# Kernel optimization log

Measured on AMD Instinct MI355X. Metric: run time of the kernel, lower is better.

The kernel has to match this reference:

```python
import jax, jax.numpy as jnp
import numpy as np

EMA_BETA = 0.9
NUM_HEADS = 16

def causal_prefix_ema(x, beta):
    # x: [b, t, d]; s_t = beta*s_{t-1} + (1-beta)*x_t, s_{-1}=0
    def step(s, xt):
        s = beta * s + (1.0 - beta) * xt
        return s, s
    s0 = jnp.zeros_like(x[:, 0, :])
    _, ys = jax.lax.scan(step, s0, jnp.swapaxes(x, 0, 1))  # [t, b, d]
    return jnp.swapaxes(ys, 0, 1)

def setup_inputs() -> dict:
    key = jax.random.key(0)
    ks = jax.random.split(key, 9)
    b, t, d = 2, 1024, 2048
    sc = lambda fan_in: 1.0 / np.sqrt(fan_in)
    return {
        "x": jax.random.normal(ks[0], (b, t, d), jnp.float32),
        "l3_memory": jax.random.normal(ks[1], (b, 1, d), jnp.float32),
        "wq": jax.random.normal(ks[2], (d, d), jnp.float32) * sc(d),
        "wk": jax.random.normal(ks[3], (d, d), jnp.float32) * sc(d),
        "wv": jax.random.normal(ks[4], (d, d), jnp.float32) * sc(d),
        "wo": jax.random.normal(ks[5], (d, d), jnp.float32) * sc(d),
        "rw1": jax.random.normal(ks[6], (d // 2, d), jnp.float32) * sc(d),
        "rb1": jnp.zeros((d // 2,), jnp.float32),
        "rw2": jax.random.normal(ks[7], (3, d // 2), jnp.float32) * sc(d // 2),
        "rb2": jnp.zeros((3,), jnp.float32),
    }

def reference(x, l3_memory, wq, wk, wv, wo, rw1, rb1, rw2, rb2):
    b, t, d = x.shape
    h = NUM_HEADS
    dh = d // h
    scale = 1.0 / np.sqrt(dh)

    q = x @ wq.T                                   # [b,t,d]
    l1 = x
    l2 = causal_prefix_ema(x, EMA_BETA)            # [b,t,d]
    l3 = jnp.broadcast_to(l3_memory, (b, t, d))    # repeat retrieval memory to length t

    # router: MLP(Q) -> softmax over 3 levels
    hdn = jax.nn.silu(q @ rw1.T + rb1)
    lam = jax.nn.softmax(hdn @ rw2.T + rb2, axis=-1)  # [b,t,3]

    fused = lam[..., 0:1] * l1 + lam[..., 1:2] * l2 + lam[..., 2:3] * l3

    def heads(y):
        return jnp.swapaxes(y.reshape(b, t, h, dh), 1, 2)  # [b,h,t,dh]

    qh = heads(q)
    kh = heads(fused @ wk.T)
    vh = heads(fused @ wv.T)

    scores = jnp.einsum("bhqd,bhkd->bhqk", qh, kh) * scale
    causal = jnp.tril(jnp.ones((t, t), bool))
    scores = jnp.where(causal, scores, jnp.finfo(scores.dtype).min)
    attn = jax.nn.softmax(scores, axis=-1)
    out = jnp.einsum("bhqk,bhkd->bhqd", attn, vh)

    out = jnp.swapaxes(out, 1, 2).reshape(b, t, d) @ wo.T
    return (out, kh, vh, lam)
```

## Files before the change

kernel.cpp:

```cpp
#include <hip/hip_runtime.h>
#include <hip/hip_bf16.h>
#include <math.h>

#define B_  2
#define T_  1024
#define D_  2048
#define H_  16
#define DH_ 128
#define M_  2048
#define DR_ 1024
#define CH_  16
#define NCH_ 64

typedef __attribute__((ext_vector_type(8))) short short8;
typedef __attribute__((ext_vector_type(4))) short sh4;
typedef __attribute__((ext_vector_type(4))) float f32x4;

__device__ __forceinline__ void gld16(const __hip_bfloat16* g, __hip_bfloat16* l) {
  __builtin_amdgcn_global_load_lds(
      (const __attribute__((address_space(1))) unsigned int*)g,
      (__attribute__((address_space(3))) unsigned int*)l, 16, 0, 0);
}

template<int BM, int CMODE, bool SILU>
__global__ __launch_bounds__(256)
void gemm_mfma(const __hip_bfloat16* __restrict__ A,
               const __hip_bfloat16* __restrict__ Bm,
               const float* __restrict__ bias,
               float* __restrict__ C, __hip_bfloat16* __restrict__ Cb,
               float* __restrict__ C2, __hip_bfloat16* __restrict__ Cb2,
               int M, int N, int K)
{
  constexpr int NI = BM / 32;
  constexpr int AC = BM / 64;
  __shared__ __hip_bfloat16 As[2][2][BM * 32];
  __shared__ __hip_bfloat16 Bs[2][2][128 * 32];
  const int tid  = threadIdx.x;
  const int wave = tid >> 6;
  const int lane = tid & 63;
  const int m0 = blockIdx.y * BM;
  const int n0 = blockIdx.x * 128;
  const int wm = (wave >> 1) * (BM / 2);
  const int wn = (wave & 1) * 64;

  const int srow = lane >> 2;
  const int scol = (lane & 3) * 8;
  const __hip_bfloat16* Ag = A  + (size_t)(m0 + wave * (BM / 4) + srow) * K + scol;
  const __hip_bfloat16* Bg = Bm + (size_t)(n0 + wave * 32 + srow) * K + scol;

  const int fr = lane & 15;
  const int fk = (lane >> 4) * 8;

  f32x4 acc[NI][4];
  #pragma unroll
  for (int i = 0; i < NI; ++i)
    #pragma unroll
    for (int j = 0; j < 4; ++j) acc[i][j] = (f32x4)0.f;

  auto stage = [&](int bf, int k0) {
    #pragma unroll
    for (int h = 0; h < 2; ++h) {
      #pragma unroll
      for (int c = 0; c < AC; ++c)
        gld16(Ag + k0 + h * 32 + (size_t)(c * 16) * K,
              &As[bf][h][(wave * (BM / 4) + c * 16) * 32]);
      #pragma unroll
      for (int c = 0; c < 2; ++c)
        gld16(Bg + k0 + h * 32 + (size_t)(c * 16) * K,
              &Bs[bf][h][(wave * 32 + c * 16) * 32]);
    }
  };

  stage(0, 0);
  __syncthreads();
  int cur = 0;
  for (int k0 = 0; k0 < K; k0 += 64) {
    if (k0 + 64 < K) stage(cur ^ 1, k0 + 64);
    #pragma unroll
    for (int h = 0; h < 2; ++h) {
      short8 af[NI], bfr[4];
      #pragma unroll
      for (int i = 0; i < NI; ++i)
        af[i]  = *(const short8*)&As[cur][h][(wm + i * 16 + fr) * 32 + fk];
      #pragma unroll
      for (int j = 0; j < 4; ++j)
        bfr[j] = *(const short8*)&Bs[cur][h][(wn + j * 16 + fr) * 32 + fk];
      #pragma unroll
      for (int i = 0; i < NI; ++i)
        #pragma unroll
        for (int j = 0; j < 4; ++j)
          acc[i][j] = __builtin_amdgcn_mfma_f32_16x16x32_bf16(af[i], bfr[j], acc[i][j], 0, 0, 0);
    }
    __syncthreads();
    cur ^= 1;
  }

  #pragma unroll
  for (int i = 0; i < NI; ++i) {
    #pragma unroll
    for (int j = 0; j < 4; ++j) {
      const int row0 = m0 + wm + i * 16 + (lane >> 4) * 4;
      const int col  = n0 + wn + j * 16 + (lane & 15);
      float vr[4];
      #pragma unroll
      for (int r = 0; r < 4; ++r) {
        float v = acc[i][j][r];
        if (bias) v += bias[col];
        if (SILU) v = v / (1.f + __expf(-v));
        vr[r] = v;
      }
      if (CMODE == 0) {
        #pragma unroll
        for (int r = 0; r < 4; ++r) C[(size_t)(row0 + r) * N + col] = vr[r];
      } else if (CMODE == 1) {
        #pragma unroll
        for (int r = 0; r < 4; ++r) Cb[(size_t)(row0 + r) * N + col] = __float2bfloat16(vr[r]);
      } else {
        const int bb = row0 >> 10, t0v = row0 & 1023;
        if (col < D_) {
          const int hh = col >> 7, dd = col & 127;
          #pragma unroll
          for (int r = 0; r < 4; ++r) {
            const size_t idx = (((size_t)(bb * H_ + hh)) * T_ + t0v + r) * DH_ + dd;
            C[idx] = vr[r];
            Cb[idx] = __float2bfloat16(vr[r]);
          }
        } else {
          const int c2 = col - D_;
          const int hh = c2 >> 7, dd = c2 & 127;
          #pragma unroll
          for (int r = 0; r < 4; ++r)
            C2[(((size_t)(bb * H_ + hh)) * T_ + t0v + r) * DH_ + dd] = vr[r];
          __hip_bfloat16 tmp[4];
          #pragma unroll
          for (int r = 0; r < 4; ++r) tmp[r] = __float2bfloat16(vr[r]);
          *(sh4*)(Cb2 + (((size_t)(bb * H_ + hh)) * DH_ + dd) * T_ + t0v) = *(const sh4*)tmp;
        }
      }
    }
  }
}

__global__ __launch_bounds__(256)
void prep_all(const float* __restrict__ x, __hip_bfloat16* __restrict__ xb,
              float* __restrict__ l2, float* __restrict__ lf,
              const float* __restrict__ s1, const float* __restrict__ s2,
              const float* __restrict__ s3, const float* __restrict__ s4,
              const float* __restrict__ s5,
              __hip_bfloat16* d1, __hip_bfloat16* d2, __hip_bfloat16* d3,
              __hip_bfloat16* d4, __hip_bfloat16* d5,
              int n1, int n2, int n3, int n4, int n5)
{
  if (blockIdx.y == 0) {
    const int bid = blockIdx.x;
    if (bid >= 256) return;
    const int dblk = bid & 1;
    const int ch   = (bid >> 1) & 63;
    const int b    = bid >> 7;
    const int t0 = ch * CH_;
    const int d  = dblk * 1024 + threadIdx.x * 4;
    const float* xp = x  + (size_t)b * T_ * D_ + d;
    float*       lp = l2 + (size_t)b * T_ * D_ + d;
    __hip_bfloat16* xo = xb + (size_t)b * T_ * D_ + d;
    float4 s = make_float4(0.f, 0.f, 0.f, 0.f);
    #pragma unroll 4
    for (int t = t0; t < t0 + CH_; ++t) {
      float4 v = *(const float4*)(xp + (size_t)t * D_);
      __hip_bfloat16 tmp[4] = {__float2bfloat16(v.x), __float2bfloat16(v.y),
                               __float2bfloat16(v.z), __float2bfloat16(v.w)};
      *(sh4*)(xo + (size_t)t * D_) = *(const sh4*)tmp;
      s.x = 0.9f * s.x + 0.1f * v.x;
      s.y = 0.9f * s.y + 0.1f * v.y;
      s.z = 0.9f * s.z + 0.1f * v.z;
      s.w = 0.9f * s.w + 0.1f * v.w;
      *(float4*)(lp + (size_t)t * D_) = s;
    }
    *(float4*)(lf + ((size_t)b * NCH_ + ch) * D_ + d) = s;
    return;
  }
  const float* s; __hip_bfloat16* d; int n;
  switch (blockIdx.y) {
    case 1: s = s1; d = d1; n = n1; break;
    case 2: s = s2; d = d2; n = n2; break;
    case 3: s = s3; d = d3; n = n3; break;
    case 4: s = s4; d = d4; n = n4; break;
    default: s = s5; d = d5; n = n5; break;
  }
  const int i = (blockIdx.x * 256 + threadIdx.x) * 8;
  if (i < n) {
    float4 a = *(const float4*)(s + i);
    float4 b = *(const float4*)(s + i + 4);
    __hip_bfloat16 t[8] = {__float2bfloat16(a.x), __float2bfloat16(a.y),
                           __float2bfloat16(a.z), __float2bfloat16(a.w),
                           __float2bfloat16(b.x), __float2bfloat16(b.y),
                           __float2bfloat16(b.z), __float2bfloat16(b.w)};
    *(short8*)(d + i) = *(const short8*)t;
  }
}

__global__ __launch_bounds__(256)
void ema_carry_scan(const float* __restrict__ lf, float* __restrict__ carry)
{
  const int wid  = (blockIdx.x * 256 + threadIdx.x) >> 6;
  const int lane = threadIdx.x & 63;
  const int b = wid >> 11, d = wid & 2047;
  float S = lf[((size_t)b * NCH_ + lane) * D_ + d];
  float p = 0.18530201888518416f;
  #pragma unroll
  for (int off = 1; off < 64; off <<= 1) {
    float Su = __shfl_up(S, off);
    float pu = __shfl_up(p, off);
    if (lane >= off) { S = S + p * Su; p = p * pu; }
  }
  float c = __shfl_up(S, 1);
  if (lane == 0) c = 0.f;
  carry[((size_t)b * NCH_ + lane) * D_ + d] = c;
}

__global__ __launch_bounds__(256)
void fuse_router(const float* __restrict__ x, const float* __restrict__ l2,
                 const float* __restrict__ l3m, const float* __restrict__ hdn,
                 const float* __restrict__ rw2, const float* __restrict__ rb2,
                 const float* __restrict__ carry, float* __restrict__ lam,
                 __hip_bfloat16* __restrict__ fb)
{
  __shared__ float lamS[8][3];
  const int tid = threadIdx.x;
  const int g = tid >> 5, l32 = tid & 31;
  const int m = blockIdx.x * 8 + g;
  const float* hp = hdn + (size_t)m * DR_;
  float s0 = 0.f, s1 = 0.f, s2 = 0.f;
  #pragma unroll
  for (int it = 0; it < 8; ++it) {
    const int k = l32 * 4 + it * 128;
    float4 h4 = *(const float4*)(hp + k);
    float4 w0 = *(const float4*)(rw2 + k);
    float4 w1 = *(const float4*)(rw2 + DR_ + k);
    float4 w2 = *(const float4*)(rw2 + 2 * DR_ + k);
    s0 += h4.x * w0.x + h4.y * w0.y + h4.z * w0.z + h4.w * w0.w;
    s1 += h4.x * w1.x + h4.y * w1.y + h4.z * w1.z + h4.w * w1.w;
    s2 += h4.x * w2.x + h4.y * w2.y + h4.z * w2.z + h4.w * w2.w;
  }
  #pragma unroll
  for (int off = 16; off > 0; off >>= 1) {
    s0 += __shfl_xor(s0, off);
    s1 += __shfl_xor(s1, off);
    s2 += __shfl_xor(s2, off);
  }
  if (l32 == 0) {
    s0 += rb2[0]; s1 += rb2[1]; s2 += rb2[2];
    float mx = fmaxf(s0, fmaxf(s1, s2));
    float e0 = __expf(s0 - mx), e1 = __expf(s1 - mx), e2 = __expf(s2 - mx);
    float inv = 1.f / (e0 + e1 + e2);
    lam[(size_t)m * 3 + 0] = e0 * inv;
    lam[(size_t)m * 3 + 1] = e1 * inv;
    lam[(size_t)m * 3 + 2] = e2 * inv;
    lamS[g][0] = e0 * inv; lamS[g][1] = e1 * inv; lamS[g][2] = e2 * inv;
  }
  __syncthreads();

  const int c = tid * 8;
  #pragma unroll
  for (int r = 0; r < 8; ++r) {
    const int mm = blockIdx.x * 8 + r;
    const int bb = mm >> 10, tt = mm & 1023;
    const int ch = tt >> 4, off = tt & 15;
    const float pw = __expf((float)(off + 1) * -0.105360515657f);
    const float u0 = lamS[r][0], u1 = lamS[r][1], u2 = lamS[r][2];
    const float* xp = x   + (size_t)mm * D_ + c;
    const float* ep = l2  + (size_t)mm * D_ + c;
    const float* gp = l3m + (size_t)bb * D_ + c;
    const float* cp = carry + ((size_t)bb * NCH_ + ch) * D_ + c;
    __hip_bfloat16 tmp[8];
    #pragma unroll
    for (int q = 0; q < 2; ++q) {
      float4 xv = *(const float4*)(xp + q * 4);
      float4 ev = *(const float4*)(ep + q * 4);
      float4 gv = *(const float4*)(gp + q * 4);
      float4 cv = *(const float4*)(cp + q * 4);
      tmp[q * 4 + 0] = __float2bfloat16(u0 * xv.x + u1 * (ev.x + pw * cv.x) + u2 * gv.x);
      tmp[q * 4 + 1] = __float2bfloat16(u0 * xv.y + u1 * (ev.y + pw * cv.y) + u2 * gv.y);
      tmp[q * 4 + 2] = __float2bfloat16(u0 * xv.z + u1 * (ev.z + pw * cv.z) + u2 * gv.z);
      tmp[q * 4 + 3] = __float2bfloat16(u0 * xv.w + u1 * (ev.w + pw * cv.w) + u2 * gv.w);
    }
    *(short8*)(fb + (size_t)mm * D_ + c) = *(const short8*)tmp;
  }
}

__global__ __launch_bounds__(256)
void flash_mfma(const __hip_bfloat16* __restrict__ qg,
                const __hip_bfloat16* __restrict__ kg,
                const __hip_bfloat16* __restrict__ vg,
                __hip_bfloat16* __restrict__ og)
{
  __shared__ __hip_bfloat16 Ks[2][64 * 136];
  __shared__ __hip_bfloat16 Vt[2][128 * 72];
  __shared__ __hip_bfloat16 Ps[64 * 72];
  const int tid  = threadIdx.x;
  const int wave = tid >> 6, lane = tid & 63;
  const int L    = blockIdx.x;
  const int halfg = L >> 8, idx = L & 255;
  const int bh = (idx >> 4) | (halfg << 4);
  const int qt = halfg ? (15 - (idx & 15)) : (idx & 15);
  const int b = bh >> 4, h = bh & 15;
  const int q0 = qt * 64;
  const int lo = lane & 15, hi = lane >> 4;

  short8 aq[4];
  {
    const __hip_bfloat16* qsrc = qg + (size_t)(b * T_ + q0 + wave * 16 + lo) * D_ + h * DH_;
    #pragma unroll
    for (int kk = 0; kk < 4; ++kk)
      aq[kk] = *(const short8*)(qsrc + kk * 32 + hi * 8);
  }

  f32x4 oacc[8];
  #pragma unroll
  for (int i = 0; i < 8; ++i) oacc[i] = (f32x4)0.f;
  float mrow[4] = {-INFINITY, -INFINITY, -INFINITY, -INFINITY};
  float lrow[4] = {0.f, 0.f, 0.f, 0.f};

  const __hip_bfloat16* kbp = kg + (size_t)bh * T_ * DH_;
  const __hip_bfloat16* vbp = vg + (size_t)bh * DH_ * T_;
  const float scale = 0.08838834764831845f;

  short8 kreg[4], vreg[4];
  auto load_tile = [&](int k0) {
    #pragma unroll
    for (int i = 0; i < 4; ++i) {
      const int ci = tid + 256 * i;
      const int r = ci >> 4, j = ci & 15;
      kreg[i] = *(const short8*)(kbp + (size_t)(k0 + r) * DH_ + j * 8);
      const int dd = ci >> 3, j2 = ci & 7;
      vreg[i] = *(const short8*)(vbp + (size_t)dd * T_ + k0 + j2 * 8);
    }
  };
  auto write_lds = [&](int bf) {
    #pragma unroll
    for (int i = 0; i < 4; ++i) {
      const int ci = tid + 256 * i;
      const int r = ci >> 4, j = ci & 15;
      *(short8*)&Ks[bf][r * 136 + j * 8] = kreg[i];
      const int dd = ci >> 3, j2 = ci & 7;
      *(short8*)&Vt[bf][dd * 72 + j2 * 8] = vreg[i];
    }
  };

  load_tile(0);
  write_lds(0);
  if (qt > 0) load_tile(64);
  __syncthreads();

  for (int kt = 0; kt <= qt; ++kt) {
    const int cur = kt & 1;
    f32x4 sc[4];
    __builtin_amdgcn_s_setprio(1);
    #pragma unroll
    for (int nt = 0; nt < 4; ++nt) {
      sc[nt] = (f32x4)0.f;
      #pragma unroll
      for (int kk = 0; kk < 4; ++kk) {
        short8 bk = *(const short8*)&Ks[cur][(nt * 16 + lo) * 136 + kk * 32 + hi * 8];
        sc[nt] = __builtin_amdgcn_mfma_f32_16x16x32_bf16(aq[kk], bk, sc[nt], 0, 0, 0);
      }
    }
    __builtin_amdgcn_s_setprio(0);
    #pragma unroll
    for (int nt = 0; nt < 4; ++nt)
      #pragma unroll
      for (int r = 0; r < 4; ++r) sc[nt][r] *= scale;
    if (kt == qt) {
      const int qrow = q0 + wave * 16 + hi * 4;
      #pragma unroll
      for (int nt = 0; nt < 4; ++nt) {
        const int key = qt * 64 + nt * 16 + lo;
        #pragma unroll
        for (int r = 0; r < 4; ++r)
          if (key > qrow + r) sc[nt][r] = -1e30f;
      }
    }
    float alpha[4];
    #pragma unroll
    for (int r = 0; r < 4; ++r) {
      float mx = fmaxf(fmaxf(sc[0][r], sc[1][r]), fmaxf(sc[2][r], sc[3][r]));
      mx = fmaxf(mx, __shfl_xor(mx, 1));
      mx = fmaxf(mx, __shfl_xor(mx, 2));
      mx = fmaxf(mx, __shfl_xor(mx, 4));
      mx = fmaxf(mx, __shfl_xor(mx, 8));
      const float nm = fmaxf(mrow[r], mx);
      alpha[r] = __expf(mrow[r] - nm);
      mrow[r] = nm;
      float ls = 0.f;
      #pragma unroll
      for (int nt = 0; nt < 4; ++nt) {
        float p = __expf(sc[nt][r] - nm);
        sc[nt][r] = p;
        ls += p;
      }
      ls += __shfl_xor(ls, 1);
      ls += __shfl_xor(ls, 2);
      ls += __shfl_xor(ls, 4);
      ls += __shfl_xor(ls, 8);
      lrow[r] = lrow[r] * alpha[r] + ls;
    }
    #pragma unroll
    for (int nt = 0; nt < 4; ++nt)
      #pragma unroll
      for (int r = 0; r < 4; ++r)
        Ps[(wave * 16 + hi * 4 + r) * 72 + nt * 16 + lo] = __float2bfloat16(sc[nt][r]);
    #pragma unroll
    for (int n2 = 0; n2 < 8; ++n2)
      #pragma unroll
      for (int r = 0; r < 4; ++r) oacc[n2][r] *= alpha[r];
    short8 ap[2];
    #pragma unroll
    for (int k2 = 0; k2 < 2; ++k2)
      ap[k2] = *(const short8*)&Ps[(wave * 16 + lo) * 72 + k2 * 32 + hi * 8];
    __builtin_amdgcn_s_setprio(1);
    #pragma unroll
    for (int n2 = 0; n2 < 8; ++n2) {
      #pragma unroll
      for (int k2 = 0; k2 < 2; ++k2) {
        short8 bv = *(const short8*)&Vt[cur][(n2 * 16 + lo) * 72 + k2 * 32 + hi * 8];
        oacc[n2] = __builtin_amdgcn_mfma_f32_16x16x32_bf16(ap[k2], bv, oacc[n2], 0, 0, 0);
      }
    }
    __builtin_amdgcn_s_setprio(0);
    if (kt < qt) {
      write_lds(cur ^ 1);
      if (kt + 1 < qt) load_tile((kt + 2) * 64);
    }
    __syncthreads();
  }

  float inv[4];
  #pragma unroll
  for (int r = 0; r < 4; ++r) inv[r] = 1.f / lrow[r];
  __hip_bfloat16* od = og + (size_t)(b * T_ + q0 + wave * 16 + hi * 4) * D_ + h * DH_;
  #pragma unroll
  for (int n2 = 0; n2 < 8; ++n2)
    #pragma unroll
    for (int r = 0; r < 4; ++r)
      od[(size_t)r * D_ + n2 * 16 + lo] = __float2bfloat16(oacc[n2][r] * inv[r]);
}

extern "C" void kernel_launch(void* const* d_in, const int* in_sizes, int n_in,
                              void* d_out, int out_size, void* d_ws, size_t ws_size,
                              hipStream_t stream)
{
  const float* x   = (const float*)d_in[0];
  const float* l3m = (const float*)d_in[1];
  const float* wq  = (const float*)d_in[2];
  const float* wk  = (const float*)d_in[3];
  const float* wv  = (const float*)d_in[4];
  const float* wo  = (const float*)d_in[5];
  const float* rw1 = (const float*)d_in[6];
  const float* rb1 = (const float*)d_in[7];
  const float* rw2 = (const float*)d_in[8];
  const float* rb2 = (const float*)d_in[9];

  float* out = (float*)d_out;
  float* kh  = out + 4194304;
  float* vh  = out + 8388608;
  float* lam = out + 12582912;

  char* wsb = (char*)d_ws;
  float*          l2_f32 = (float*)(wsb);
  float*          hdn    = (float*)(wsb + (16u << 20));
  __hip_bfloat16* wkb    = (__hip_bfloat16*)(wsb + (24u << 20));
  __hip_bfloat16* wvb    = (__hip_bfloat16*)(wsb + (32u << 20));
  __hip_bfloat16* wob    = (__hip_bfloat16*)(wsb + (40u << 20));
  __hip_bfloat16* fusedb = (__hip_bfloat16*)(wsb + (48u << 20));
  __hip_bfloat16* attnb  = (__hip_bfloat16*)(wsb + (56u << 20));
  __hip_bfloat16* khb    = (__hip_bfloat16*)(wsb + (64u << 20));
  __hip_bfloat16* vtb    = (__hip_bfloat16*)(wsb + (72u << 20));
  float*          carry  = (float*)attnb;
  float*          lf     = (float*)(wsb + (57u << 20));
  __hip_bfloat16* wqb  = (__hip_bfloat16*)kh;
  __hip_bfloat16* rw1b = (__hip_bfloat16*)kh + 4194304;
  __hip_bfloat16* xb   = (__hip_bfloat16*)vh;
  __hip_bfloat16* qb   = (__hip_bfloat16*)out;

  dim3 blk(256);

  prep_all<<<dim3(2048, 6), blk, 0, stream>>>(x, xb, l2_f32, lf,
                                              wq, wk, wv, wo, rw1,
                                              wqb, wkb, wvb, wob, rw1b,
                                              D_ * D_, D_ * D_, D_ * D_, D_ * D_, DR_ * D_);
  ema_carry_scan<<<dim3(1024), blk, 0, stream>>>(lf, carry);
  gemm_mfma<64, 1, false><<<dim3(16, 32), blk, 0, stream>>>(xb, wqb, nullptr, nullptr, qb, nullptr, nullptr, M_, D_, D_);
  gemm_mfma<64, 0, true><<<dim3(8, 32), blk, 0, stream>>>(qb, rw1b, rb1, hdn, nullptr, nullptr, nullptr, M_, DR_, D_);
  fuse_router<<<dim3(256), blk, 0, stream>>>(x, l2_f32, l3m, hdn, rw2, rb2, carry, lam, fusedb);
  gemm_mfma<128, 4, false><<<dim3(32, 16), blk, 0, stream>>>(fusedb, wkb, nullptr, kh, khb, vh, vtb, M_, 2 * D_, D_);
  flash_mfma<<<dim3(512), blk, 0, stream>>>(qb, khb, vtb, attnb);
  gemm_mfma<64, 0, false><<<dim3(16, 32), blk, 0, stream>>>(attnb, wob, nullptr, out, nullptr, nullptr, nullptr, M_, D_, D_);
}
```

Before: 343.7 us.

## Fold EMA carry scan into fuse_router and remap GEMM blocks across XCDs

Drops the separate ema_carry_scan launch. Each fuse_router block now computes its chunk carry directly, as a sequential weighted sum over all previous chunk totals. This removes one kernel launch and the carry buffer round trip, but later chunks do up to 63 extra global loads per thread. The GEMM kernel also remaps the linear block index so that consecutive blocks are interleaved across the 8 XCDs, aiming for better L2 reuse of shared A/B tiles.

```diff
diff --git a/kernel.cpp b/kernel.cpp
--- a/kernel.cpp
+++ b/kernel.cpp
@@ -38,8 +38,17 @@
   const int tid  = threadIdx.x;
   const int wave = tid >> 6;
   const int lane = tid & 63;
-  const int m0 = blockIdx.y * BM;
-  const int n0 = blockIdx.x * 128;
+
+  const int gx = gridDim.x, gy = gridDim.y;
+  const int nwg = gx * gy;
+  int lb = blockIdx.y * gx + blockIdx.x;
+  lb = (lb & 7) * (nwg >> 3) + (lb >> 3);
+  const int ly = __popc(gy - 1);
+  const int by = lb & (gy - 1);
+  const int bx = lb >> ly;
+
+  const int m0 = by * BM;
+  const int n0 = bx * 128;
   const int wm = (wave >> 1) * (BM / 2);
   const int wn = (wave & 1) * 64;
 
@@ -199,29 +208,10 @@
 }
 
 __global__ __launch_bounds__(256)
-void ema_carry_scan(const float* __restrict__ lf, float* __restrict__ carry)
-{
-  const int wid  = (blockIdx.x * 256 + threadIdx.x) >> 6;
-  const int lane = threadIdx.x & 63;
-  const int b = wid >> 11, d = wid & 2047;
-  float S = lf[((size_t)b * NCH_ + lane) * D_ + d];
-  float p = 0.18530201888518416f;
-  #pragma unroll
-  for (int off = 1; off < 64; off <<= 1) {
-    float Su = __shfl_up(S, off);
-    float pu = __shfl_up(p, off);
-    if (lane >= off) { S = S + p * Su; p = p * pu; }
-  }
-  float c = __shfl_up(S, 1);
-  if (lane == 0) c = 0.f;
-  carry[((size_t)b * NCH_ + lane) * D_ + d] = c;
-}
-
-__global__ __launch_bounds__(256)
 void fuse_router(const float* __restrict__ x, const float* __restrict__ l2,
                  const float* __restrict__ l3m, const float* __restrict__ hdn,
                  const float* __restrict__ rw2, const float* __restrict__ rb2,
-                 const float* __restrict__ carry, float* __restrict__ lam,
+                 const float* __restrict__ lf, float* __restrict__ lam,
                  __hip_bfloat16* __restrict__ fb)
 {
   __shared__ float lamS[8][3];
@@ -257,31 +247,53 @@
     lam[(size_t)m * 3 + 2] = e2 * inv;
     lamS[g][0] = e0 * inv; lamS[g][1] = e1 * inv; lamS[g][2] = e2 * inv;
   }
+
+  const int m0b = blockIdx.x * 8;
+  const int bb  = m0b >> 10;
+  const int ch  = (m0b & 1023) >> 4;
+  const int c   = tid * 8;
+  float4 cv0 = make_float4(0.f, 0.f, 0.f, 0.f);
+  float4 cv1 = make_float4(0.f, 0.f, 0.f, 0.f);
+  {
+    float w = 1.f;
+    for (int j = ch - 1; j >= 0; --j) {
+      const float* lp = lf + ((size_t)bb * NCH_ + j) * D_ + c;
+      float4 a0 = *(const float4*)(lp);
+      float4 a1 = *(const float4*)(lp + 4);
+      cv0.x += w * a0.x; cv0.y += w * a0.y; cv0.z += w * a0.z; cv0.w += w * a0.w;
+      cv1.x += w * a1.x; cv1.y += w * a1.y; cv1.z += w * a1.z; cv1.w += w * a1.w;
+      w *= 0.18530201888518416f;
+    }
+  }
   __syncthreads();
 
-  const int c = tid * 8;
+  const int base = m0b & 15;
   #pragma unroll
   for (int r = 0; r < 8; ++r) {
-    const int mm = blockIdx.x * 8 + r;
-    const int bb = mm >> 10, tt = mm & 1023;
-    const int ch = tt >> 4, off = tt & 15;
-    const float pw = __expf((float)(off + 1) * -0.105360515657f);
+    const int mm = m0b + r;
+    const float pw = __expf((float)(base + r + 1) * -0.105360515657f);
     const float u0 = lamS[r][0], u1 = lamS[r][1], u2 = lamS[r][2];
     const float* xp = x   + (size_t)mm * D_ + c;
     const float* ep = l2  + (size_t)mm * D_ + c;
     const float* gp = l3m + (size_t)bb * D_ + c;
-    const float* cp = carry + ((size_t)bb * NCH_ + ch) * D_ + c;
     __hip_bfloat16 tmp[8];
-    #pragma unroll
-    for (int q = 0; q < 2; ++q) {
-      float4 xv = *(const float4*)(xp + q * 4);
-      float4 ev = *(const float4*)(ep + q * 4);
-      float4 gv = *(const float4*)(gp + q * 4);
-      float4 cv = *(const float4*)(cp + q * 4);
-      tmp[q * 4 + 0] = __float2bfloat16(u0 * xv.x + u1 * (ev.x + pw * cv.x) + u2 * gv.x);
-      tmp[q * 4 + 1] = __float2bfloat16(u0 * xv.y + u1 * (ev.y + pw * cv.y) + u2 * gv.y);
-      tmp[q * 4 + 2] = __float2bfloat16(u0 * xv.z + u1 * (ev.z + pw * cv.z) + u2 * gv.z);
-      tmp[q * 4 + 3] = __float2bfloat16(u0 * xv.w + u1 * (ev.w + pw * cv.w) + u2 * gv.w);
+    {
+      float4 xv = *(const float4*)(xp);
+      float4 ev = *(const float4*)(ep);
+      float4 gv = *(const float4*)(gp);
+      tmp[0] = __float2bfloat16(u0 * xv.x + u1 * (ev.x + pw * cv0.x) + u2 * gv.x);
+      tmp[1] = __float2bfloat16(u0 * xv.y + u1 * (ev.y + pw * cv0.y) + u2 * gv.y);
+      tmp[2] = __float2bfloat16(u0 * xv.z + u1 * (ev.z + pw * cv0.z) + u2 * gv.z);
+      tmp[3] = __float2bfloat16(u0 * xv.w + u1 * (ev.w + pw * cv0.w) + u2 * gv.w);
+    }
+    {
+      float4 xv = *(const float4*)(xp + 4);
+      float4 ev = *(const float4*)(ep + 4);
+      float4 gv = *(const float4*)(gp + 4);
+      tmp[4] = __float2bfloat16(u0 * xv.x + u1 * (ev.x + pw * cv1.x) + u2 * gv.x);
+      tmp[5] = __float2bfloat16(u0 * xv.y + u1 * (ev.y + pw * cv1.y) + u2 * gv.y);
+      tmp[6] = __float2bfloat16(u0 * xv.z + u1 * (ev.z + pw * cv1.z) + u2 * gv.z);
+      tmp[7] = __float2bfloat16(u0 * xv.w + u1 * (ev.w + pw * cv1.w) + u2 * gv.w);
     }
     *(short8*)(fb + (size_t)mm * D_ + c) = *(const short8*)tmp;
   }
@@ -474,7 +486,6 @@
   __hip_bfloat16* attnb  = (__hip_bfloat16*)(wsb + (56u << 20));
   __hip_bfloat16* khb    = (__hip_bfloat16*)(wsb + (64u << 20));
   __hip_bfloat16* vtb    = (__hip_bfloat16*)(wsb + (72u << 20));
-  float*          carry  = (float*)attnb;
   float*          lf     = (float*)(wsb + (57u << 20));
   __hip_bfloat16* wqb  = (__hip_bfloat16*)kh;
   __hip_bfloat16* rw1b = (__hip_bfloat16*)kh + 4194304;
@@ -487,10 +498,9 @@
                                               wq, wk, wv, wo, rw1,
                                               wqb, wkb, wvb, wob, rw1b,
                                               D_ * D_, D_ * D_, D_ * D_, D_ * D_, DR_ * D_);
-  ema_carry_scan<<<dim3(1024), blk, 0, stream>>>(lf, carry);
   gemm_mfma<64, 1, false><<<dim3(16, 32), blk, 0, stream>>>(xb, wqb, nullptr, nullptr, qb, nullptr, nullptr, M_, D_, D_);
   gemm_mfma<64, 0, true><<<dim3(8, 32), blk, 0, stream>>>(qb, rw1b, rb1, hdn, nullptr, nullptr, nullptr, M_, DR_, D_);
-  fuse_router<<<dim3(256), blk, 0, stream>>>(x, l2_f32, l3m, hdn, rw2, rb2, carry, lam, fusedb);
+  fuse_router<<<dim3(256), blk, 0, stream>>>(x, l2_f32, l3m, hdn, rw2, rb2, lf, lam, fusedb);
   gemm_mfma<128, 4, false><<<dim3(32, 16), blk, 0, stream>>>(fusedb, wkb, nullptr, kh, khb, vh, vtb, M_, 2 * D_, D_);
   flash_mfma<<<dim3(512), blk, 0, stream>>>(qb, khb, vtb, attnb);
   gemm_mfma<64, 0, false><<<dim3(16, 32), blk, 0, stream>>>(attnb, wob, nullptr, out, nullptr, nullptr, nullptr, M_, D_, D_);
```

Result: no change. 346.6 us (+0.9%).
